# Performance work log

Measured on AMD Instinct MI355X. Metric: run time of the kernel, lower is better.

The kernel has to match this reference:

```python
import jax, jax.numpy as jnp
import numpy as np

B, S, D = 2, 2048, 512
H, HD = 8, 64  # num_heads, head_size; all_head_size = H*HD = 512


def setup_inputs() -> dict:
    key = jax.random.key(0)
    ks = jax.random.split(key, 11)
    sc = 0.02
    return {
        "query": jax.random.normal(ks[0], (B, S, D), jnp.float32),
        "key": jax.random.normal(ks[1], (B, S, D), jnp.float32),
        "value": jax.random.normal(ks[2], (B, S, D), jnp.float32),
        "Wq": jax.random.normal(ks[3], (D, H * HD), jnp.float32) * sc,
        "bq": jnp.zeros((H * HD,), jnp.float32),
        "Wk": jax.random.normal(ks[4], (D, H * HD), jnp.float32) * sc,
        "bk": jnp.zeros((H * HD,), jnp.float32),
        "Wv": jax.random.normal(ks[5], (D, H * HD), jnp.float32) * sc,
        "bv": jnp.zeros((H * HD,), jnp.float32),
        "Wo": jax.random.normal(ks[6], (H * HD, D), jnp.float32) * sc,
        "bo": jnp.zeros((D,), jnp.float32),
    }


def _split_heads(x):
    b, s, _ = x.shape
    return x.reshape(b, s, H, HD).transpose(0, 2, 1, 3)  # [B,H,S,HD]


def reference(query, key, value, Wq, bq, Wk, bk, Wv, bv, Wo, bo):
    q = _split_heads(query @ Wq + bq)
    k = _split_heads(key @ Wk + bk)
    v = _split_heads(value @ Wv + bv)
    scores = jnp.einsum("bhqd,bhkd->bhqk", q, k) / jnp.sqrt(jnp.asarray(HD, q.dtype))
    probs = jax.nn.softmax(scores, axis=-1)  # dropout rate 0.0, inference
    ctx = jnp.einsum("bhqk,bhkd->bhqd", probs, v)
    ctx = ctx.transpose(0, 2, 1, 3).reshape(query.shape[0], -1, H * HD)
    return ctx @ Wo + bo
```

## Files before the change

### kernel.cpp

```cpp
#include <hip/hip_runtime.h>
#include <math.h>

#define BATCH 2
#define SEQ 2048
#define DMODEL 512
#define NH 8
#define HDIM 64
#define MTOT (BATCH * SEQ)
#define QSIZE (BATCH * NH * SEQ * HDIM)
#define WSIZE (DMODEL * DMODEL)

typedef __attribute__((ext_vector_type(8))) short bf16x8;
typedef __attribute__((ext_vector_type(4))) float f32x4;

__device__ inline unsigned short f2bf(float f) {
    union { float f; unsigned u; } v; v.f = f;
    unsigned u = v.u;
    u += 0x7fffu + ((u >> 16) & 1u);
    return (unsigned short)(u >> 16);
}
__device__ inline unsigned pack2(float lo, float hi) {
    return (unsigned)f2bf(lo) | ((unsigned)f2bf(hi) << 16);
}

#define LSTR 72

#define WS_Q   ((size_t)0)
#define WS_K   ((size_t)QSIZE)
#define WS_V   (2 * (size_t)QSIZE)
#define WS_CTX (3 * (size_t)QSIZE)
#define WS_WT  (4 * (size_t)QSIZE)
#define WS_ABF (4 * (size_t)QSIZE + 4 * (size_t)WSIZE)

__global__ __launch_bounds__(256) void wt_prep_kernel(
    const float* __restrict__ Wq, const float* __restrict__ Wk,
    const float* __restrict__ Wv, const float* __restrict__ Wo,
    unsigned short* __restrict__ wt)
{
    const int z = blockIdx.z;
    const float* W = (z == 0) ? Wq : (z == 1) ? Wk : (z == 2) ? Wv : Wo;
    unsigned short* Wt = wt + (size_t)z * WSIZE;

    __shared__ float T[32][33];
    const int tid = threadIdx.x;
    const int k0 = blockIdx.x * 32, n0 = blockIdx.y * 32;

    {
        int r = tid >> 3, c = (tid & 7) * 4;
        float4 v = *(const float4*)&W[(size_t)(k0 + r) * DMODEL + n0 + c];
        T[r][c + 0] = v.x; T[r][c + 1] = v.y; T[r][c + 2] = v.z; T[r][c + 3] = v.w;
    }
    __syncthreads();
    {
        int n = tid >> 3, c = (tid & 7) * 4;
        uint2 o;
        o.x = pack2(T[c + 0][n], T[c + 1][n]);
        o.y = pack2(T[c + 2][n], T[c + 3][n]);
        *(uint2*)&Wt[(size_t)(n0 + n) * DMODEL + k0 + c] = o;
    }
}

__global__ __launch_bounds__(256) void inp_prep_kernel(
    const float* __restrict__ qin, const float* __restrict__ kin,
    const float* __restrict__ vin, unsigned short* __restrict__ abf)
{
    const int z = blockIdx.y;
    const float* src = (z == 0) ? qin : (z == 1) ? kin : vin;
    unsigned short* dst = abf + (size_t)z * QSIZE;

    const size_t i = ((size_t)blockIdx.x * 256 + threadIdx.x) * 8;
    float4 f0 = *(const float4*)(src + i);
    float4 f1 = *(const float4*)(src + i + 4);
    uint4 o;
    o.x = pack2(f0.x, f0.y); o.y = pack2(f0.z, f0.w);
    o.z = pack2(f1.x, f1.y); o.w = pack2(f1.z, f1.w);
    *(uint4*)(dst + i) = o;
}

__global__ __launch_bounds__(256) void qkv_mfma_kernel(
    unsigned short* __restrict__ ws,
    const float* __restrict__ bq, const float* __restrict__ bk,
    const float* __restrict__ bv)
{
    const int which = blockIdx.z;
    const unsigned short* A  = ws + WS_ABF + (size_t)which * QSIZE;
    const unsigned short* Wt = ws + WS_WT + (size_t)which * WSIZE;
    const float* bias = (which == 0) ? bq : (which == 1) ? bk : bv;
    unsigned short* out = ws + (size_t)which * QSIZE;

    __shared__ __align__(16) short As[128][LSTR];
    __shared__ __align__(16) short Bs[128][LSTR];

    const int tid = threadIdx.x;
    const int lane = tid & 63, wave = tid >> 6;
    const int lrow = lane & 15, quad = lane >> 4;
    const int m0 = blockIdx.y * 128, n0 = blockIdx.x * 128;

    const int sr = tid >> 1;
    const int sh = (tid & 1) * 32;

    f32x4 acc[2][8];
    #pragma unroll
    for (int i = 0; i < 2; ++i)
        #pragma unroll
        for (int n = 0; n < 8; ++n) acc[i][n] = f32x4{0.f, 0.f, 0.f, 0.f};

    for (int k0 = 0; k0 < DMODEL; k0 += 64) {
        __syncthreads();
        {
            const unsigned short* ap = A + (size_t)(m0 + sr) * DMODEL + k0 + sh;
            uint4 a0 = *(const uint4*)(ap + 0),  a1 = *(const uint4*)(ap + 8);
            uint4 a2 = *(const uint4*)(ap + 16), a3 = *(const uint4*)(ap + 24);
            *(uint4*)&As[sr][sh + 0]  = a0;
            *(uint4*)&As[sr][sh + 8]  = a1;
            *(uint4*)&As[sr][sh + 16] = a2;
            *(uint4*)&As[sr][sh + 24] = a3;
        }
        {
            const unsigned short* wp = Wt + (size_t)(n0 + sr) * DMODEL + k0 + sh;
            uint4 b0 = *(const uint4*)(wp + 0),  b1 = *(const uint4*)(wp + 8);
            uint4 b2 = *(const uint4*)(wp + 16), b3 = *(const uint4*)(wp + 24);
            *(uint4*)&Bs[sr][sh + 0]  = b0;
            *(uint4*)&Bs[sr][sh + 8]  = b1;
            *(uint4*)&Bs[sr][sh + 16] = b2;
            *(uint4*)&Bs[sr][sh + 24] = b3;
        }
        __syncthreads();
        #pragma unroll
        for (int s = 0; s < 2; ++s) {
            bf16x8 af[2];
            #pragma unroll
            for (int i = 0; i < 2; ++i)
                af[i] = *(const bf16x8*)&As[wave * 32 + i * 16 + lrow][s * 32 + quad * 8];
            #pragma unroll
            for (int n = 0; n < 8; ++n) {
                bf16x8 bf = *(const bf16x8*)&Bs[n * 16 + lrow][s * 32 + quad * 8];
                acc[0][n] = __builtin_amdgcn_mfma_f32_16x16x32_bf16(af[0], bf, acc[0][n], 0, 0, 0);
                acc[1][n] = __builtin_amdgcn_mfma_f32_16x16x32_bf16(af[1], bf, acc[1][n], 0, 0, 0);
            }
        }
    }

    if (which < 2) {
        const float scale = (which == 0) ? 0.125f : 1.0f;
        #pragma unroll
        for (int n = 0; n < 8; ++n) {
            const int col = n0 + n * 16 + lrow;
            const int h_ = col >> 6, hd_ = col & 63;
            const float bv_ = bias[col];
            #pragma unroll
            for (int i = 0; i < 2; ++i) {
                #pragma unroll
                for (int r = 0; r < 4; ++r) {
                    const int m = m0 + wave * 32 + i * 16 + quad * 4 + r;
                    const int b_ = m >> 11, s_ = m & (SEQ - 1);
                    const float v = (acc[i][n][r] + bv_) * scale;
                    out[((size_t)((b_ * NH + h_) * SEQ + s_)) * HDIM + hd_] = f2bf(v);
                }
            }
        }
    } else {
        #pragma unroll
        for (int n = 0; n < 8; ++n) {
            const int col = n0 + n * 16 + lrow;
            const int h_ = col >> 6, hd_ = col & 63;
            const float bv_ = bias[col];
            #pragma unroll
            for (int i = 0; i < 2; ++i) {
                const int m = m0 + wave * 32 + i * 16 + quad * 4;
                const int b_ = m >> 11, s_ = m & (SEQ - 1);
                uint2 o;
                o.x = pack2(acc[i][n][0] + bv_, acc[i][n][1] + bv_);
                o.y = pack2(acc[i][n][2] + bv_, acc[i][n][3] + bv_);
                *(uint2*)&out[((size_t)((b_ * NH + h_) * HDIM + hd_)) * SEQ + s_] = o;
            }
        }
    }
}

__global__ __launch_bounds__(256) void attn_mfma_kernel(
    const unsigned short* __restrict__ ws, unsigned short* __restrict__ ctx)
{
    const unsigned short* Q = ws + WS_Q;
    const unsigned short* K = ws + WS_K;
    const unsigned short* V = ws + WS_V;

    __shared__ __align__(16) short Ks[64][LSTR];
    __shared__ __align__(16) short Vt[64][LSTR];
    __shared__ __align__(16) short Ps[64][LSTR];

    const int bh = blockIdx.x;
    const int q0 = blockIdx.y * 64;
    const int tid = threadIdx.x;
    const int lane = tid & 63, wave = tid >> 6;
    const int lrow = lane & 15, quad = lane >> 4;
    const size_t base = (size_t)bh * SEQ * HDIM;

    const unsigned short* qrow = Q + base + (size_t)(q0 + wave * 16 + lrow) * HDIM;
    const bf16x8 qb0 = *(const bf16x8*)(qrow + quad * 8);
    const bf16x8 qb1 = *(const bf16x8*)(qrow + 32 + quad * 8);

    float m_prev = -1e30f, l_run = 0.f;
    f32x4 oacc[4];
    #pragma unroll
    for (int n = 0; n < 4; ++n) oacc[n] = f32x4{0.f, 0.f, 0.f, 0.f};

    const int kr = tid >> 2, kc = (tid & 3) * 16;
    const int vr = tid >> 2, vq = (tid & 3) * 16;

    for (int kt = 0; kt < SEQ; kt += 64) {
        __syncthreads();
        {
            const unsigned short* kp = K + base + (size_t)(kt + kr) * HDIM + kc;
            uint4 k0 = *(const uint4*)kp;
            uint4 k1 = *(const uint4*)(kp + 8);
            *(uint4*)&Ks[kr][kc]     = k0;
            *(uint4*)&Ks[kr][kc + 8] = k1;
        }
        {
            const unsigned short* vp = V + base + (size_t)vr * SEQ + kt + vq;
            uint4 v0 = *(const uint4*)vp;
            uint4 v1 = *(const uint4*)(vp + 8);
            *(uint4*)&Vt[vr][vq]     = v0;
            *(uint4*)&Vt[vr][vq + 8] = v1;
        }
        __syncthreads();

        f32x4 st[4];
        #pragma unroll
        for (int n = 0; n < 4; ++n) {
            bf16x8 ka0 = *(const bf16x8*)&Ks[n * 16 + lrow][quad * 8];
            bf16x8 ka1 = *(const bf16x8*)&Ks[n * 16 + lrow][32 + quad * 8];
            f32x4 z = f32x4{0.f, 0.f, 0.f, 0.f};
            z = __builtin_amdgcn_mfma_f32_16x16x32_bf16(ka0, qb0, z, 0, 0, 0);
            z = __builtin_amdgcn_mfma_f32_16x16x32_bf16(ka1, qb1, z, 0, 0, 0);
            st[n] = z;
        }

        float tmax = st[0][0];
        #pragma unroll
        for (int n = 0; n < 4; ++n)
            #pragma unroll
            for (int r = 0; r < 4; ++r) tmax = fmaxf(tmax, st[n][r]);
        tmax = fmaxf(tmax, __shfl_xor(tmax, 16));
        tmax = fmaxf(tmax, __shfl_xor(tmax, 32));

        const float mnew = fmaxf(m_prev, tmax);
        const float alpha = __expf(m_prev - mnew);
        float p[4][4];
        float tsum = 0.f;
        #pragma unroll
        for (int n = 0; n < 4; ++n)
            #pragma unroll
            for (int r = 0; r < 4; ++r) {
                p[n][r] = __expf(st[n][r] - mnew);
                tsum += p[n][r];
            }
        tsum += __shfl_xor(tsum, 16);
        tsum += __shfl_xor(tsum, 32);
        l_run = l_run * alpha + tsum;
        m_prev = mnew;
        #pragma unroll
        for (int n = 0; n < 4; ++n) {
            oacc[n][0] *= alpha; oacc[n][1] *= alpha;
            oacc[n][2] *= alpha; oacc[n][3] *= alpha;
        }
        #pragma unroll
        for (int n = 0; n < 4; ++n) {
            uint2 o;
            o.x = pack2(p[n][0], p[n][1]);
            o.y = pack2(p[n][2], p[n][3]);
            *(uint2*)&Ps[wave * 16 + lrow][n * 16 + quad * 4] = o;
        }

        bf16x8 pb0 = *(const bf16x8*)&Ps[wave * 16 + lrow][quad * 8];
        bf16x8 pb1 = *(const bf16x8*)&Ps[wave * 16 + lrow][32 + quad * 8];
        #pragma unroll
        for (int n = 0; n < 4; ++n) {
            bf16x8 va0 = *(const bf16x8*)&Vt[n * 16 + lrow][quad * 8];
            bf16x8 va1 = *(const bf16x8*)&Vt[n * 16 + lrow][32 + quad * 8];
            oacc[n] = __builtin_amdgcn_mfma_f32_16x16x32_bf16(va0, pb0, oacc[n], 0, 0, 0);
            oacc[n] = __builtin_amdgcn_mfma_f32_16x16x32_bf16(va1, pb1, oacc[n], 0, 0, 0);
        }
    }

    const int b_ = bh >> 3, h_ = bh & 7;
    const float inv = 1.f / l_run;
    const int qg = q0 + wave * 16 + lrow;
    unsigned short* crow = ctx + ((size_t)(b_ * SEQ + qg)) * DMODEL + h_ * HDIM;
    #pragma unroll
    for (int n = 0; n < 4; ++n) {
        uint2 o;
        o.x = pack2(oacc[n][0] * inv, oacc[n][1] * inv);
        o.y = pack2(oacc[n][2] * inv, oacc[n][3] * inv);
        *(uint2*)&crow[n * 16 + quad * 4] = o;
    }
}

__global__ __launch_bounds__(256) void out_proj_mfma_kernel(
    const unsigned short* __restrict__ ws, const float* __restrict__ bo,
    float* __restrict__ out)
{
    const unsigned short* ctx = ws + WS_CTX;
    const unsigned short* Wt  = ws + WS_WT + 3 * (size_t)WSIZE;

    __shared__ __align__(16) short As[128][LSTR];
    __shared__ __align__(16) short Bs[64][LSTR];

    const int tid = threadIdx.x;
    const int lane = tid & 63, wave = tid >> 6;
    const int lrow = lane & 15, quad = lane >> 4;
    const int m0 = blockIdx.y * 128, n0 = blockIdx.x * 64;

    const int sr = tid >> 1, sh = (tid & 1) * 32;
    const int br = tid >> 2, bqr = (tid & 3) * 16;

    f32x4 acc[2][4];
    #pragma unroll
    for (int i = 0; i < 2; ++i)
        #pragma unroll
        for (int n = 0; n < 4; ++n) acc[i][n] = f32x4{0.f, 0.f, 0.f, 0.f};

    for (int k0 = 0; k0 < DMODEL; k0 += 64) {
        __syncthreads();
        {
            const unsigned short* ap = ctx + (size_t)(m0 + sr) * DMODEL + k0 + sh;
            uint4 c0 = *(const uint4*)(ap + 0),  c1 = *(const uint4*)(ap + 8);
            uint4 c2 = *(const uint4*)(ap + 16), c3 = *(const uint4*)(ap + 24);
            *(uint4*)&As[sr][sh + 0]  = c0;
            *(uint4*)&As[sr][sh + 8]  = c1;
            *(uint4*)&As[sr][sh + 16] = c2;
            *(uint4*)&As[sr][sh + 24] = c3;
        }
        {
            const unsigned short* wp = Wt + (size_t)(n0 + br) * DMODEL + k0 + bqr;
            uint4 b0 = *(const uint4*)wp;
            uint4 b1 = *(const uint4*)(wp + 8);
            *(uint4*)&Bs[br][bqr]     = b0;
            *(uint4*)&Bs[br][bqr + 8] = b1;
        }
        __syncthreads();
        #pragma unroll
        for (int s = 0; s < 2; ++s) {
            bf16x8 af[2];
            #pragma unroll
            for (int i = 0; i < 2; ++i)
                af[i] = *(const bf16x8*)&As[wave * 32 + i * 16 + lrow][s * 32 + quad * 8];
            #pragma unroll
            for (int n = 0; n < 4; ++n) {
                bf16x8 bf = *(const bf16x8*)&Bs[n * 16 + lrow][s * 32 + quad * 8];
                acc[0][n] = __builtin_amdgcn_mfma_f32_16x16x32_bf16(af[0], bf, acc[0][n], 0, 0, 0);
                acc[1][n] = __builtin_amdgcn_mfma_f32_16x16x32_bf16(af[1], bf, acc[1][n], 0, 0, 0);
            }
        }
    }

    #pragma unroll
    for (int n = 0; n < 4; ++n) {
        const int col = n0 + n * 16 + lrow;
        const float bv_ = bo[col];
        #pragma unroll
        for (int i = 0; i < 2; ++i) {
            #pragma unroll
            for (int r = 0; r < 4; ++r) {
                const int m = m0 + wave * 32 + i * 16 + quad * 4 + r;
                out[(size_t)m * DMODEL + col] = acc[i][n][r] + bv_;
            }
        }
    }
}

extern "C" void kernel_launch(void* const* d_in, const int* in_sizes, int n_in,
                              void* d_out, int out_size, void* d_ws, size_t ws_size,
                              hipStream_t stream)
{
    const float* qin = (const float*)d_in[0];
    const float* kin = (const float*)d_in[1];
    const float* vin = (const float*)d_in[2];
    const float* Wq  = (const float*)d_in[3];
    const float* bq  = (const float*)d_in[4];
    const float* Wk  = (const float*)d_in[5];
    const float* bk  = (const float*)d_in[6];
    const float* Wv  = (const float*)d_in[7];
    const float* bv  = (const float*)d_in[8];
    const float* Wo  = (const float*)d_in[9];
    const float* bo  = (const float*)d_in[10];

    unsigned short* ws = (unsigned short*)d_ws;
    float* out = (float*)d_out;

    dim3 gw(DMODEL / 32, DMODEL / 32, 4);
    wt_prep_kernel<<<gw, 256, 0, stream>>>(Wq, Wk, Wv, Wo, ws + WS_WT);

    dim3 gi(QSIZE / (256 * 8), 3);
    inp_prep_kernel<<<gi, 256, 0, stream>>>(qin, kin, vin, ws + WS_ABF);

    dim3 gp(DMODEL / 128, MTOT / 128, 3);
    qkv_mfma_kernel<<<gp, 256, 0, stream>>>(ws, bq, bk, bv);

    dim3 ga(BATCH * NH, SEQ / 64);
    attn_mfma_kernel<<<ga, 256, 0, stream>>>(ws, ws + WS_CTX);

    dim3 go(DMODEL / 64, MTOT / 128);
    out_proj_mfma_kernel<<<go, 256, 0, stream>>>(ws, bo, out);
}
```

Measured before the change: 172.1 us.

## Split attention KV range across two wave groups, add lazy rescale and hw bf16 pack

The attention block grows to 512 threads. Each group of four waves handles half of the key sequence and keeps its own online-softmax state, and the two partial results are merged through shared memory at the end. This doubles the waves available to hide latency per query tile. The online-softmax rescale is skipped unless the tile max exceeds the running max by more than 8, which removes exp and multiply work on most iterations. bf16 packing now uses the v_cvt_pk_bf16_f32 instruction instead of software rounding. The cost is more shared memory per block, lower block-level occupancy, and an extra merge phase with synchronisation.

```diff
diff --git a/kernel.cpp b/kernel.cpp
--- a/kernel.cpp
+++ b/kernel.cpp
@@ -20,7 +20,9 @@
     return (unsigned short)(u >> 16);
 }
 __device__ inline unsigned pack2(float lo, float hi) {
-    return (unsigned)f2bf(lo) | ((unsigned)f2bf(hi) << 16);
+    unsigned r;
+    asm("v_cvt_pk_bf16_f32 %0, %1, %2" : "=v"(r) : "v"(lo), "v"(hi));
+    return r;
 }
 
 #define LSTR 72
@@ -178,25 +180,29 @@
     }
 }
 
-__global__ __launch_bounds__(256) void attn_mfma_kernel(
+#define HSEQ (SEQ / 2)
+#define OSTR 68
+
+__global__ __launch_bounds__(512) void attn_mfma_kernel(
     const unsigned short* __restrict__ ws, unsigned short* __restrict__ ctx)
 {
     const unsigned short* Q = ws + WS_Q;
     const unsigned short* K = ws + WS_K;
     const unsigned short* V = ws + WS_V;
 
-    __shared__ __align__(16) short Ks[64][LSTR];
-    __shared__ __align__(16) short Vt[64][LSTR];
-    __shared__ __align__(16) short Ps[64][LSTR];
+    __shared__ __align__(16) short Ks[2][64][LSTR];
+    __shared__ __align__(16) short Vt[2][64][LSTR];
+    __shared__ __align__(16) short Ps[2][64][LSTR];
 
     const int bh = blockIdx.x;
     const int q0 = blockIdx.y * 64;
     const int tid = threadIdx.x;
     const int lane = tid & 63, wave = tid >> 6;
+    const int half = wave >> 2, w4 = wave & 3;
     const int lrow = lane & 15, quad = lane >> 4;
     const size_t base = (size_t)bh * SEQ * HDIM;
 
-    const unsigned short* qrow = Q + base + (size_t)(q0 + wave * 16 + lrow) * HDIM;
+    const unsigned short* qrow = Q + base + (size_t)(q0 + w4 * 16 + lrow) * HDIM;
     const bf16x8 qb0 = *(const bf16x8*)(qrow + quad * 8);
     const bf16x8 qb1 = *(const bf16x8*)(qrow + 32 + quad * 8);
 
@@ -205,32 +211,33 @@
     #pragma unroll
     for (int n = 0; n < 4; ++n) oacc[n] = f32x4{0.f, 0.f, 0.f, 0.f};
 
-    const int kr = tid >> 2, kc = (tid & 3) * 16;
-    const int vr = tid >> 2, vq = (tid & 3) * 16;
-
-    for (int kt = 0; kt < SEQ; kt += 64) {
-        __syncthreads();
-        {
-            const unsigned short* kp = K + base + (size_t)(kt + kr) * HDIM + kc;
+    const int t = tid & 255;
+    const int kr = t >> 2, kc = (t & 3) * 16;
+    const int ktbase = half * HSEQ;
+
+    for (int kt = 0; kt < HSEQ; kt += 64) {
+        __syncthreads();
+        {
+            const unsigned short* kp = K + base + (size_t)(ktbase + kt + kr) * HDIM + kc;
             uint4 k0 = *(const uint4*)kp;
             uint4 k1 = *(const uint4*)(kp + 8);
-            *(uint4*)&Ks[kr][kc]     = k0;
-            *(uint4*)&Ks[kr][kc + 8] = k1;
-        }
-        {
-            const unsigned short* vp = V + base + (size_t)vr * SEQ + kt + vq;
+            *(uint4*)&Ks[half][kr][kc]     = k0;
+            *(uint4*)&Ks[half][kr][kc + 8] = k1;
+        }
+        {
+            const unsigned short* vp = V + base + (size_t)kr * SEQ + ktbase + kt + kc;
             uint4 v0 = *(const uint4*)vp;
             uint4 v1 = *(const uint4*)(vp + 8);
-            *(uint4*)&Vt[vr][vq]     = v0;
-            *(uint4*)&Vt[vr][vq + 8] = v1;
+            *(uint4*)&Vt[half][kr][kc]     = v0;
+            *(uint4*)&Vt[half][kr][kc + 8] = v1;
         }
         __syncthreads();
 
         f32x4 st[4];
         #pragma unroll
         for (int n = 0; n < 4; ++n) {
-            bf16x8 ka0 = *(const bf16x8*)&Ks[n * 16 + lrow][quad * 8];
-            bf16x8 ka1 = *(const bf16x8*)&Ks[n * 16 + lrow][32 + quad * 8];
+            bf16x8 ka0 = *(const bf16x8*)&Ks[half][n * 16 + lrow][quad * 8];
+            bf16x8 ka1 = *(const bf16x8*)&Ks[half][n * 16 + lrow][32 + quad * 8];
             f32x4 z = f32x4{0.f, 0.f, 0.f, 0.f};
             z = __builtin_amdgcn_mfma_f32_16x16x32_bf16(ka0, qb0, z, 0, 0, 0);
             z = __builtin_amdgcn_mfma_f32_16x16x32_bf16(ka1, qb1, z, 0, 0, 0);
@@ -245,55 +252,85 @@
         tmax = fmaxf(tmax, __shfl_xor(tmax, 16));
         tmax = fmaxf(tmax, __shfl_xor(tmax, 32));
 
-        const float mnew = fmaxf(m_prev, tmax);
-        const float alpha = __expf(m_prev - mnew);
+        if (!__all(tmax <= m_prev + 8.f)) {
+            const float mnew = fmaxf(m_prev, tmax);
+            const float alpha = __expf(m_prev - mnew);
+            l_run *= alpha;
+            #pragma unroll
+            for (int n = 0; n < 4; ++n) {
+                oacc[n][0] *= alpha; oacc[n][1] *= alpha;
+                oacc[n][2] *= alpha; oacc[n][3] *= alpha;
+            }
+            m_prev = mnew;
+        }
+
         float p[4][4];
         float tsum = 0.f;
         #pragma unroll
         for (int n = 0; n < 4; ++n)
             #pragma unroll
             for (int r = 0; r < 4; ++r) {
-                p[n][r] = __expf(st[n][r] - mnew);
+                p[n][r] = __expf(st[n][r] - m_prev);
                 tsum += p[n][r];
             }
         tsum += __shfl_xor(tsum, 16);
         tsum += __shfl_xor(tsum, 32);
-        l_run = l_run * alpha + tsum;
-        m_prev = mnew;
-        #pragma unroll
-        for (int n = 0; n < 4; ++n) {
-            oacc[n][0] *= alpha; oacc[n][1] *= alpha;
-            oacc[n][2] *= alpha; oacc[n][3] *= alpha;
-        }
+        l_run += tsum;
+
         #pragma unroll
         for (int n = 0; n < 4; ++n) {
             uint2 o;
             o.x = pack2(p[n][0], p[n][1]);
             o.y = pack2(p[n][2], p[n][3]);
-            *(uint2*)&Ps[wave * 16 + lrow][n * 16 + quad * 4] = o;
-        }
-
-        bf16x8 pb0 = *(const bf16x8*)&Ps[wave * 16 + lrow][quad * 8];
-        bf16x8 pb1 = *(const bf16x8*)&Ps[wave * 16 + lrow][32 + quad * 8];
+            *(uint2*)&Ps[half][w4 * 16 + lrow][n * 16 + quad * 4] = o;
+        }
+
+        bf16x8 pb0 = *(const bf16x8*)&Ps[half][w4 * 16 + lrow][quad * 8];
+        bf16x8 pb1 = *(const bf16x8*)&Ps[half][w4 * 16 + lrow][32 + quad * 8];
         #pragma unroll
         for (int n = 0; n < 4; ++n) {
-            bf16x8 va0 = *(const bf16x8*)&Vt[n * 16 + lrow][quad * 8];
-            bf16x8 va1 = *(const bf16x8*)&Vt[n * 16 + lrow][32 + quad * 8];
+            bf16x8 va0 = *(const bf16x8*)&Vt[half][n * 16 + lrow][quad * 8];
+            bf16x8 va1 = *(const bf16x8*)&Vt[half][n * 16 + lrow][32 + quad * 8];
             oacc[n] = __builtin_amdgcn_mfma_f32_16x16x32_bf16(va0, pb0, oacc[n], 0, 0, 0);
             oacc[n] = __builtin_amdgcn_mfma_f32_16x16x32_bf16(va1, pb1, oacc[n], 0, 0, 0);
         }
     }
 
-    const int b_ = bh >> 3, h_ = bh & 7;
-    const float inv = 1.f / l_run;
-    const int qg = q0 + wave * 16 + lrow;
-    unsigned short* crow = ctx + ((size_t)(b_ * SEQ + qg)) * DMODEL + h_ * HDIM;
-    #pragma unroll
-    for (int n = 0; n < 4; ++n) {
-        uint2 o;
-        o.x = pack2(oacc[n][0] * inv, oacc[n][1] * inv);
-        o.y = pack2(oacc[n][2] * inv, oacc[n][3] * inv);
-        *(uint2*)&crow[n * 16 + quad * 4] = o;
+    __syncthreads();
+    float* Obuf = (float*)&Ks[0][0][0];
+    float* Mbuf = (float*)&Ps[0][0][0];
+
+    if (half == 1) {
+        float* ob = Obuf + (size_t)w4 * (16 * OSTR) + (size_t)lrow * OSTR;
+        #pragma unroll
+        for (int n = 0; n < 4; ++n)
+            *(f32x4*)&ob[n * 16 + quad * 4] = oacc[n];
+        if (quad == 0) {
+            Mbuf[w4 * 16 + lrow]      = m_prev;
+            Mbuf[64 + w4 * 16 + lrow] = l_run;
+        }
+    }
+    __syncthreads();
+    if (half == 0) {
+        const float m1 = Mbuf[w4 * 16 + lrow];
+        const float l1 = Mbuf[64 + w4 * 16 + lrow];
+        const float M  = fmaxf(m_prev, m1);
+        const float a0 = __expf(m_prev - M), a1 = __expf(m1 - M);
+        const float inv = 1.f / (l_run * a0 + l1 * a1);
+        const float s0 = a0 * inv, s1 = a1 * inv;
+        const float* ob = Obuf + (size_t)w4 * (16 * OSTR) + (size_t)lrow * OSTR;
+
+        const int b_ = bh >> 3, h_ = bh & 7;
+        const int qg = q0 + w4 * 16 + lrow;
+        unsigned short* crow = ctx + ((size_t)(b_ * SEQ + qg)) * DMODEL + h_ * HDIM;
+        #pragma unroll
+        for (int n = 0; n < 4; ++n) {
+            f32x4 o1 = *(const f32x4*)&ob[n * 16 + quad * 4];
+            uint2 o;
+            o.x = pack2(oacc[n][0] * s0 + o1[0] * s1, oacc[n][1] * s0 + o1[1] * s1);
+            o.y = pack2(oacc[n][2] * s0 + o1[2] * s1, oacc[n][3] * s0 + o1[3] * s1);
+            *(uint2*)&crow[n * 16 + quad * 4] = o;
+        }
     }
 }
 
@@ -399,7 +436,7 @@
     qkv_mfma_kernel<<<gp, 256, 0, stream>>>(ws, bq, bk, bv);
 
     dim3 ga(BATCH * NH, SEQ / 64);
-    attn_mfma_kernel<<<ga, 256, 0, stream>>>(ws, ws + WS_CTX);
+    attn_mfma_kernel<<<ga, 512, 0, stream>>>(ws, ws + WS_CTX);
 
     dim3 go(DMODEL / 64, MTOT / 128);
     out_proj_mfma_kernel<<<go, 256, 0, stream>>>(ws, bo, out);
```

Measured after the change: 157.9 us. 8.2% less time.
